# Performance work log

Hardware: AMD Instinct MI355X
Metric: run time of the kernel (lower is better)

The kernel has to match this reference:

```python
import jax, jax.numpy as jnp
import numpy as np

N = 100000        # nodes
E = 1600000       # directed edges (before self loops)
F = 128           # input node features
H1, H2, H3 = 64, 32, 16
G = 64            # graphs in batch
EPS = 1e-5
NEG_SLOPE = 0.2


def setup_inputs():
    key = jax.random.key(0)
    ks = jax.random.split(key, 16)
    def rn(k, shape, scale=1.0):
        return jax.random.normal(k, shape, dtype=jnp.float32) * scale
    inp = {}
    inp['x'] = rn(ks[0], (N, F))
    inp['edge_index'] = jax.random.randint(ks[1], (2, E), 0, N)
    inp['batch'] = jnp.sort(jax.random.randint(ks[2], (N,), 0, G))
    dims = [(F, H1), (H1, H2), (H2, H3)]
    i = 3
    for li, (fi, fo) in enumerate(dims, start=1):
        s = 1.0 / np.sqrt(fi)
        kk = jax.random.split(ks[i], 3)
        inp[f'Wl{li}'] = rn(kk[0], (fi, fo), s)
        inp[f'bl{li}'] = jnp.zeros((fo,), jnp.float32)
        inp[f'Wr{li}'] = rn(kk[1], (fi, fo), s)
        inp[f'br{li}'] = jnp.zeros((fo,), jnp.float32)
        inp[f'att{li}'] = rn(kk[2], (fo,), 1.0 / np.sqrt(fo))
        inp[f'bias{li}'] = jnp.zeros((fo,), jnp.float32)
        inp[f'gamma{li}'] = jnp.ones((fo,), jnp.float32)
        inp[f'beta{li}'] = jnp.zeros((fo,), jnp.float32)
        i += 1
    inp['linW'] = rn(ks[i], (H3, 1), 0.25)
    inp['linb'] = jnp.zeros((1,), jnp.float32)
    return inp


def _gatv2(x, Wl, bl, Wr, br, att, bias, src, dst):
    # PyG GATv2Conv, heads=1: e_ij = a^T LeakyReLU(Wl x_j + Wr x_i)
    xl = x @ Wl + bl                         # [N, H] source transform
    xr = x @ Wr + br                         # [N, H] target transform
    e = jax.nn.leaky_relu(xl[src] + xr[dst], NEG_SLOPE) @ att   # [E']
    # numerically stable segment softmax over incoming edges of dst
    emax = jax.ops.segment_max(e, dst, num_segments=N)
    w = jnp.exp(e - emax[dst])
    denom = jax.ops.segment_sum(w, dst, num_segments=N)
    alpha = w / (denom[dst] + 1e-16)         # [E']
    out = jax.ops.segment_sum(alpha[:, None] * xl[src], dst, num_segments=N)
    return out + bias


def _batchnorm(x, gamma, beta):
    mu = jnp.mean(x, axis=0)
    var = jnp.var(x, axis=0)
    return (x - mu) * jax.lax.rsqrt(var + EPS) * gamma + beta


def reference(x, edge_index, batch,
              Wl1, bl1, Wr1, br1, att1, bias1, gamma1, beta1,
              Wl2, bl2, Wr2, br2, att2, bias2, gamma2, beta2,
              Wl3, bl3, Wr3, br3, att3, bias3, gamma3, beta3,
              linW, linb):
    # add self loops once (PyG GATv2Conv default add_self_loops=True)
    loops = jnp.arange(N, dtype=edge_index.dtype)
    src = jnp.concatenate([edge_index[0], loops])
    dst = jnp.concatenate([edge_index[1], loops])

    h = _gatv2(x, Wl1, bl1, Wr1, br1, att1, bias1, src, dst)
    h = jax.nn.relu(_batchnorm(h, gamma1, beta1))
    h = _gatv2(h, Wl2, bl2, Wr2, br2, att2, bias2, src, dst)
    h = jax.nn.relu(_batchnorm(h, gamma2, beta2))
    h = _gatv2(h, Wl3, bl3, Wr3, br3, att3, bias3, src, dst)
    h = jax.nn.relu(_batchnorm(h, gamma3, beta3))

    # global mean pool over graphs
    sums = jax.ops.segment_sum(h, batch, num_segments=G)          # [G, 16]
    cnts = jax.ops.segment_sum(jnp.ones((N,), h.dtype), batch, num_segments=G)
    pooled = sums / jnp.maximum(cnts, 1.0)[:, None]
    return pooled @ linW + linb                                   # [G, 1]
```

## Files before the change

kernel.cpp:

```cpp
#include <hip/hip_runtime.h>
#include <hip/hip_bf16.h>


static constexpr int G_ = 64;

__global__ __launch_bounds__(256) void pack_w(
    const float* __restrict__ Wl, const float* __restrict__ Wr,
    const float* __restrict__ bl, const float* __restrict__ br,
    float* __restrict__ Wcat, float* __restrict__ bcat, int FI, int H) {
  int i = blockIdx.x * 256 + threadIdx.x;
  int FO = 2 * H;
  if (i < FI * FO) {
    int k = i / FO, c = i % FO;
    Wcat[i] = (c < H) ? Wl[k * H + c] : Wr[k * H + (c - H)];
  }
  if (i < FO) bcat[i] = (i < H) ? bl[i] : br[i - H];
}

template <int FI>
__global__ __launch_bounds__(256) void transpose_nf(
    const float* __restrict__ A, float* __restrict__ At, int N) {
  __shared__ float s[64][65];
  int n0 = blockIdx.x * 64, k0 = blockIdx.y * 64;
  int tid = threadIdx.x;
  for (int idx = tid; idx < 64 * 16; idx += 256) {
    int n = idx >> 4, c = idx & 15;
    float4 v = make_float4(0.f, 0.f, 0.f, 0.f);
    if (n0 + n < N)
      v = *reinterpret_cast<const float4*>(&A[(size_t)(n0 + n) * FI + k0 + c * 4]);
    s[n][c * 4 + 0] = v.x; s[n][c * 4 + 1] = v.y;
    s[n][c * 4 + 2] = v.z; s[n][c * 4 + 3] = v.w;
  }
  __syncthreads();
  for (int idx = tid; idx < 64 * 16; idx += 256) {
    int k = idx >> 4, c = idx & 15;
    int n = c * 4;
    if (n0 + n + 3 < N) {
      float4 v = make_float4(s[n][k], s[n + 1][k], s[n + 2][k], s[n + 3][k]);
      *reinterpret_cast<float4*>(&At[(size_t)(k0 + k) * N + n0 + n]) = v;
    } else {
      for (int j = 0; j < 4; j++)
        if (n0 + n + j < N) At[(size_t)(k0 + k) * N + n0 + n + j] = s[n + j][k];
    }
  }
}

__global__ __launch_bounds__(256) void edge_hist(
    const int* __restrict__ ei, int* __restrict__ deg, int E, int Etot, int N) {
  int p = blockIdx.x & 7;
  int q = blockIdx.x >> 3;
  int nbq = gridDim.x >> 3;
  float scale = 8.0f / (float)N;
  for (int i = q * 256 + threadIdx.x; i < Etot; i += nbq * 256) {
    int dst = (i < E) ? ei[E + i] : (i - E);
    int pp = min((int)((float)dst * scale), 7);
    if (pp == p) atomicAdd(&deg[dst], 1);
  }
}

__global__ __launch_bounds__(256) void scan1(
    const int* __restrict__ deg, int* __restrict__ part, int* __restrict__ bsums, int n) {
  __shared__ int ts[256];
  int t = threadIdx.x, b = blockIdx.x;
  int base = b * 1024 + t * 4;
  int d[4];
#pragma unroll
  for (int q = 0; q < 4; q++) d[q] = (base + q < n) ? deg[base + q] : 0;
  int s = d[0] + d[1] + d[2] + d[3];
  ts[t] = s;
  __syncthreads();
  for (int o = 1; o < 256; o <<= 1) {
    int v = (t >= o) ? ts[t - o] : 0;
    __syncthreads();
    ts[t] += v;
    __syncthreads();
  }
  int incl = ts[t];
  if (t == 255) bsums[b] = incl;
  int run = incl - s;
#pragma unroll
  for (int q = 0; q < 4; q++) {
    if (base + q < n) part[base + q] = run;
    run += d[q];
  }
}

__global__ void scan2(int* bsums, int nb) {
  if (threadIdx.x == 0 && blockIdx.x == 0) {
    int r = 0;
    for (int i = 0; i < nb; i++) { int t = bsums[i]; bsums[i] = r; r += t; }
  }
}

__global__ __launch_bounds__(256) void scan3(
    int* __restrict__ rp, int* __restrict__ cur, const int* __restrict__ bsums,
    int n, int Etot) {
  int i = blockIdx.x * 256 + threadIdx.x;
  if (i < n) {
    int v = rp[i] + bsums[i >> 10];
    rp[i] = v; cur[i] = v;
  }
  if (i == 0) rp[n] = Etot;
}

__global__ __launch_bounds__(256) void scatter_edges(
    const int* __restrict__ ei, int* __restrict__ cur, int* __restrict__ ssrc,
    int E, int Etot, int N) {
  int p = blockIdx.x & 7;
  int q = blockIdx.x >> 3;
  int nbq = gridDim.x >> 3;
  float scale = 8.0f / (float)N;
  for (int i = q * 256 + threadIdx.x; i < Etot; i += nbq * 256) {
    int dst = (i < E) ? ei[E + i] : (i - E);
    int pp = min((int)((float)dst * scale), 7);
    if (pp != p) continue;
    int src = (i < E) ? ei[i] : (i - E);
    int pos = atomicAdd(&cur[dst], 1);
    ssrc[pos] = src;
  }
}

template <int FI, int FO>
__global__ __launch_bounds__(256) void gemm_fmaj(
    const float* __restrict__ At, const float* __restrict__ Wcat,
    const float* __restrict__ bcat, float* __restrict__ C, int N) {
  constexpr int KC = 32;
  constexpr int HP = FO / 16;
  __shared__ float As[FI * 64];
  __shared__ float Ws[KC * FO];
  int tid = threadIdx.x;
  int ng = tid & 15, hg = tid >> 4;
  int n0 = blockIdx.x * 64;

  if (n0 + 64 <= N) {
    for (int idx = tid; idx < FI * 16; idx += 256) {
      int k = idx >> 4, c = idx & 15;
      *reinterpret_cast<float4*>(&As[k * 64 + c * 4]) =
          *reinterpret_cast<const float4*>(&At[(size_t)k * N + n0 + c * 4]);
    }
  } else {
    for (int idx = tid; idx < FI * 64; idx += 256) {
      int k = idx >> 6, nn = idx & 63;
      As[k * 64 + nn] = (n0 + nn < N) ? At[(size_t)k * N + n0 + nn] : 0.f;
    }
  }

  float acc[4][HP];
#pragma unroll
  for (int i = 0; i < 4; i++)
#pragma unroll
    for (int j = 0; j < HP; j++) acc[i][j] = 0.f;

  for (int kc = 0; kc < FI; kc += KC) {
    __syncthreads();
    for (int idx = tid; idx < KC * FO / 4; idx += 256)
      *reinterpret_cast<float4*>(&Ws[idx * 4]) =
          *reinterpret_cast<const float4*>(&Wcat[kc * FO + idx * 4]);
    __syncthreads();
#pragma unroll
    for (int kk = 0; kk < KC; kk++) {
      float a_[4];
#pragma unroll
      for (int i = 0; i < 4; i++) a_[i] = As[(kc + kk) * 64 + ng * 4 + i];
      float w_[HP];
#pragma unroll
      for (int j = 0; j < HP; j++) w_[j] = Ws[kk * FO + hg * HP + j];
#pragma unroll
      for (int i = 0; i < 4; i++)
#pragma unroll
        for (int j = 0; j < HP; j++) acc[i][j] += a_[i] * w_[j];
    }
  }

#pragma unroll
  for (int i = 0; i < 4; i++) {
    int n = n0 + ng * 4 + i;
    if (n < N) {
#pragma unroll
      for (int j = 0; j < HP; j++)
        C[(size_t)n * FO + hg * HP + j] = acc[i][j] + bcat[hg * HP + j];
    }
  }
}

__device__ __forceinline__ float lrelu02(float z) {
  return (z > 0.f) ? z : 0.2f * z;
}

template <int H, bool UN2>
__global__ __launch_bounds__(256) void gat_agg2(
    const float* __restrict__ xlr, const float* __restrict__ att,
    const float* __restrict__ bias, const int* __restrict__ rp,
    const int* __restrict__ ssrc, float* __restrict__ out, int N) {
  constexpr int L = H / 4;
  constexpr int C = 64 / L;
  int v = blockIdx.x * 4 + (threadIdx.x >> 6);
  if (v >= N) return;
  int lane = threadIdx.x & 63;
  int fl = lane % L;
  int sub = lane / L;

  const float4 xr4 = *reinterpret_cast<const float4*>(&xlr[(size_t)v * (2 * H) + H + fl * 4]);
  const float4 a4 = *reinterpret_cast<const float4*>(&att[fl * 4]);
  int beg = rp[v], end = rp[v + 1];

  float mA = -3.0e38f, dA = 0.f;
  float4 accA = make_float4(0.f, 0.f, 0.f, 0.f);
  float mB = -3.0e38f, dB = 0.f;
  float4 accB = make_float4(0.f, 0.f, 0.f, 0.f);

  constexpr int STEP = UN2 ? 2 * C : C;

  for (int j = beg + sub; j < end; j += STEP) {
    {
      int u = ssrc[j];
      float4 xl4 = *reinterpret_cast<const float4*>(&xlr[(size_t)u * (2 * H) + fl * 4]);
      float t = a4.x * lrelu02(xl4.x + xr4.x);
      t = fmaf(a4.y, lrelu02(xl4.y + xr4.y), t);
      t = fmaf(a4.z, lrelu02(xl4.z + xr4.z), t);
      t = fmaf(a4.w, lrelu02(xl4.w + xr4.w), t);
#pragma unroll
      for (int o = L / 2; o >= 1; o >>= 1) t += __shfl_xor(t, o);
      float mn = fmaxf(mA, t);
      float sc = __expf(mA - mn);
      float w = __expf(t - mn);
      dA = dA * sc + w;
      accA.x = fmaf(w, xl4.x, accA.x * sc);
      accA.y = fmaf(w, xl4.y, accA.y * sc);
      accA.z = fmaf(w, xl4.z, accA.z * sc);
      accA.w = fmaf(w, xl4.w, accA.w * sc);
      mA = mn;
    }
    if (UN2) {
      int j2 = j + C;
      if (j2 < end) {
        int u = ssrc[j2];
        float4 xl4 = *reinterpret_cast<const float4*>(&xlr[(size_t)u * (2 * H) + fl * 4]);
        float t = a4.x * lrelu02(xl4.x + xr4.x);
        t = fmaf(a4.y, lrelu02(xl4.y + xr4.y), t);
        t = fmaf(a4.z, lrelu02(xl4.z + xr4.z), t);
        t = fmaf(a4.w, lrelu02(xl4.w + xr4.w), t);
#pragma unroll
        for (int o = L / 2; o >= 1; o >>= 1) t += __shfl_xor(t, o);
        float mn = fmaxf(mB, t);
        float sc = __expf(mB - mn);
        float w = __expf(t - mn);
        dB = dB * sc + w;
        accB.x = fmaf(w, xl4.x, accB.x * sc);
        accB.y = fmaf(w, xl4.y, accB.y * sc);
        accB.z = fmaf(w, xl4.z, accB.z * sc);
        accB.w = fmaf(w, xl4.w, accB.w * sc);
        mB = mn;
      }
    }
  }

  if (UN2) {
    float mn = fmaxf(mA, mB);
    float s1 = __expf(mA - mn), s2 = __expf(mB - mn);
    dA = dA * s1 + dB * s2;
    accA.x = accA.x * s1 + accB.x * s2;
    accA.y = accA.y * s1 + accB.y * s2;
    accA.z = accA.z * s1 + accB.z * s2;
    accA.w = accA.w * s1 + accB.w * s2;
    mA = mn;
  }

#pragma unroll
  for (int o = L; o < 64; o <<= 1) {
    float mo = __shfl_xor(mA, o);
    float d2 = __shfl_xor(dA, o);
    float ax = __shfl_xor(accA.x, o);
    float ay = __shfl_xor(accA.y, o);
    float az = __shfl_xor(accA.z, o);
    float aw = __shfl_xor(accA.w, o);
    float mn = fmaxf(mA, mo);
    float s1 = __expf(mA - mn), s2 = __expf(mo - mn);
    dA = dA * s1 + d2 * s2;
    accA.x = accA.x * s1 + ax * s2;
    accA.y = accA.y * s1 + ay * s2;
    accA.z = accA.z * s1 + az * s2;
    accA.w = accA.w * s1 + aw * s2;
    mA = mn;
  }

  if (lane < L) {
    float inv = 1.f / (dA + 1e-16f);
    const float4 b4 = *reinterpret_cast<const float4*>(&bias[fl * 4]);
    float4 o4 = make_float4(fmaf(accA.x, inv, b4.x), fmaf(accA.y, inv, b4.y),
                            fmaf(accA.z, inv, b4.z), fmaf(accA.w, inv, b4.w));
    *reinterpret_cast<float4*>(&out[(size_t)v * H + fl * 4]) = o4;
  }
}

template <int H>
__global__ __launch_bounds__(256) void bn_stats(
    const float* __restrict__ X, float* __restrict__ stats, int N) {
  __shared__ float ls[256], ls2[256];
  int tid = threadIdx.x;
  int h = tid % H;
  constexpr int RPB = 256 / H;
  int r0 = blockIdx.x * RPB + tid / H;
  float s = 0.f, s2 = 0.f;
  for (int n = r0; n < N; n += gridDim.x * RPB) {
    float val = X[(size_t)n * H + h];
    s += val; s2 += val * val;
  }
  ls[tid] = s; ls2[tid] = s2;
  __syncthreads();
  if (tid < H) {
    for (int g = 1; g < RPB; g++) { s += ls[tid + g * H]; s2 += ls2[tid + g * H]; }
    atomicAdd(&stats[h], s);
    atomicAdd(&stats[H + h], s2);
  }
}

__global__ void bn_finalize(
    const float* __restrict__ stats, const float* __restrict__ gamma,
    const float* __restrict__ beta, float* __restrict__ ss, int H, int N) {
  int h = threadIdx.x;
  if (h < H) {
    float mean = stats[h] / (float)N;
    float var = stats[H + h] / (float)N - mean * mean;
    float istd = rsqrtf(var + 1e-5f);
    float sc = gamma[h] * istd;
    ss[h] = sc;
    ss[H + h] = beta[h] - mean * sc;
  }
}

template <int H>
__global__ __launch_bounds__(256) void bn_apply_T(
    const float* __restrict__ X, const float* __restrict__ ss,
    float* __restrict__ Yt, int N) {
  __shared__ float s[64][65];
  int n0 = blockIdx.x * 64;
  int tid = threadIdx.x;
  for (int idx = tid; idx < 64 * (H / 4); idx += 256) {
    int n = idx / (H / 4), c = idx % (H / 4);
    float4 v = make_float4(0.f, 0.f, 0.f, 0.f);
    if (n0 + n < N)
      v = *reinterpret_cast<const float4*>(&X[(size_t)(n0 + n) * H + c * 4]);
    s[n][c * 4 + 0] = v.x; s[n][c * 4 + 1] = v.y;
    s[n][c * 4 + 2] = v.z; s[n][c * 4 + 3] = v.w;
  }
  __syncthreads();
  for (int idx = tid; idx < H * 16; idx += 256) {
    int k = idx >> 4, c = idx & 15;
    int n = c * 4;
    float sc = ss[k], sh = ss[H + k];
    float t0 = s[n + 0][k] * sc + sh;
    float t1 = s[n + 1][k] * sc + sh;
    float t2 = s[n + 2][k] * sc + sh;
    float t3 = s[n + 3][k] * sc + sh;
    float4 v = make_float4(t0 > 0.f ? t0 : 0.f, t1 > 0.f ? t1 : 0.f,
                           t2 > 0.f ? t2 : 0.f, t3 > 0.f ? t3 : 0.f);
    if (n0 + n + 3 < N) {
      *reinterpret_cast<float4*>(&Yt[(size_t)k * N + n0 + n]) = v;
    } else {
      float tv[4] = {v.x, v.y, v.z, v.w};
      for (int j = 0; j < 4; j++)
        if (n0 + n + j < N) Yt[(size_t)k * N + n0 + n + j] = tv[j];
    }
  }
}

__global__ __launch_bounds__(256) void bn_apply_flat(
    const float* __restrict__ X, const float* __restrict__ ss,
    float* __restrict__ Y, int total) {
  int i = blockIdx.x * 256 + threadIdx.x;
  if (i < total) {
    int h = i & 15;
    float t = X[i] * ss[h] + ss[16 + h];
    Y[i] = t > 0.f ? t : 0.f;
  }
}

__global__ __launch_bounds__(256) void pool_kernel(
    const float* __restrict__ X, const int* __restrict__ batch,
    float* __restrict__ pool, float* __restrict__ cnt, int N) {
  __shared__ float lp[G_ * 16];
  __shared__ float lc[G_];
  int tid = threadIdx.x;
  for (int j = tid; j < G_ * 16; j += 256) lp[j] = 0.f;
  if (tid < G_) lc[tid] = 0.f;
  __syncthreads();
  int tot = N * 16;
  for (int i = blockIdx.x * 256 + tid; i < tot; i += gridDim.x * 256) {
    int n = i >> 4, h = i & 15;
    int g = batch[n];
    atomicAdd(&lp[g * 16 + h], X[i]);
    if (h == 0) atomicAdd(&lc[g], 1.0f);
  }
  __syncthreads();
  for (int j = tid; j < G_ * 16; j += 256) atomicAdd(&pool[j], lp[j]);
  if (tid < G_) atomicAdd(&cnt[tid], lc[tid]);
}

__global__ void final_linear(
    const float* __restrict__ pool, const float* __restrict__ cnt,
    const float* __restrict__ linW, const float* __restrict__ linb,
    float* __restrict__ out) {
  int g = threadIdx.x;
  if (g < G_) {
    float c = fmaxf(cnt[g], 1.0f);
    float acc = 0.f;
    for (int h = 0; h < 16; h++) acc += (pool[g * 16 + h] / c) * linW[h];
    out[g] = acc + linb[0];
  }
}

extern "C" void kernel_launch(void* const* d_in, const int* in_sizes, int n_in,
                              void* d_out, int out_size, void* d_ws, size_t ws_size,
                              hipStream_t stream) {
  const float* x = (const float*)d_in[0];
  const int* ei = (const int*)d_in[1];
  const int* batch = (const int*)d_in[2];
  const int N = in_sizes[0] / 128;
  const int E = in_sizes[1] / 2;
  const int Etot = E + N;

  char* wsb = (char*)d_ws;
  size_t off = 0;
  auto alloc = [&](size_t bytes) -> void* {
    void* p = wsb + off;
    off += (bytes + 255) & ~(size_t)255;
    return p;
  };
  float* R0 = (float*)alloc((size_t)128 * N * 4);
  float* R1 = (float*)alloc((size_t)128 * N * 4);
  float* R2 = (float*)alloc((size_t)64 * N * 4);
  int* deg = (int*)alloc((size_t)N * 4);
  int* row_ptr = (int*)alloc((size_t)(N + 1) * 4);
  int* cursor = (int*)alloc((size_t)N * 4);
  int* bsums = (int*)alloc(4096);
  int* ssrc = (int*)alloc((size_t)Etot * 4);
  float* Wc1 = (float*)alloc(16384 * 4);  float* bc1 = (float*)alloc(128 * 4);
  float* Wc2 = (float*)alloc(4096 * 4);   float* bc2 = (float*)alloc(64 * 4);
  float* Wc3 = (float*)alloc(1024 * 4);   float* bc3 = (float*)alloc(32 * 4);
  float* stats = (float*)alloc(128 * 4);
  float* ss = (float*)alloc(128 * 4);
  float* pool = (float*)alloc((G_ * 16 + G_) * 4);
  float* cnt = pool + G_ * 16;

  const float* Wl1 = (const float*)d_in[3];  const float* bl1 = (const float*)d_in[4];
  const float* Wr1 = (const float*)d_in[5];  const float* br1 = (const float*)d_in[6];
  const float* att1 = (const float*)d_in[7]; const float* bias1 = (const float*)d_in[8];
  const float* g1 = (const float*)d_in[9];   const float* b1 = (const float*)d_in[10];
  const float* Wl2 = (const float*)d_in[11]; const float* bl2 = (const float*)d_in[12];
  const float* Wr2 = (const float*)d_in[13]; const float* br2 = (const float*)d_in[14];
  const float* att2 = (const float*)d_in[15]; const float* bias2 = (const float*)d_in[16];
  const float* g2 = (const float*)d_in[17];  const float* b2 = (const float*)d_in[18];
  const float* Wl3 = (const float*)d_in[19]; const float* bl3 = (const float*)d_in[20];
  const float* Wr3 = (const float*)d_in[21]; const float* br3 = (const float*)d_in[22];
  const float* att3 = (const float*)d_in[23]; const float* bias3 = (const float*)d_in[24];
  const float* g3 = (const float*)d_in[25];  const float* b3 = (const float*)d_in[26];
  const float* linW = (const float*)d_in[27]; const float* linb = (const float*)d_in[28];
  float* out = (float*)d_out;

  int ntiles = (N + 63) / 64;
  int nb = (N + 1023) / 1024;
  int nnodeblk = (N + 3) / 4;

  pack_w<<<64, 256, 0, stream>>>(Wl1, Wr1, bl1, br1, Wc1, bc1, 128, 64);
  pack_w<<<16, 256, 0, stream>>>(Wl2, Wr2, bl2, br2, Wc2, bc2, 64, 32);
  pack_w<<<4, 256, 0, stream>>>(Wl3, Wr3, bl3, br3, Wc3, bc3, 32, 16);

  transpose_nf<128><<<dim3(ntiles, 2), 256, 0, stream>>>(x, R0, N);

  hipMemsetAsync(deg, 0, (size_t)N * 4, stream);
  edge_hist<<<4096, 256, 0, stream>>>(ei, deg, E, Etot, N);
  scan1<<<nb, 256, 0, stream>>>(deg, row_ptr, bsums, N);
  scan2<<<1, 64, 0, stream>>>(bsums, nb);
  scan3<<<(N + 255) / 256, 256, 0, stream>>>(row_ptr, cursor, bsums, N, Etot);
  scatter_edges<<<4096, 256, 0, stream>>>(ei, cursor, ssrc, E, Etot, N);

  gemm_fmaj<128, 128><<<ntiles, 256, 0, stream>>>(R0, Wc1, bc1, R1, N);
  gat_agg2<64, true><<<nnodeblk, 256, 0, stream>>>(R1, att1, bias1, row_ptr, ssrc, R2, N);
  hipMemsetAsync(stats, 0, 128 * 4, stream);
  bn_stats<64><<<512, 256, 0, stream>>>(R2, stats, N);
  bn_finalize<<<1, 64, 0, stream>>>(stats, g1, b1, ss, 64, N);
  bn_apply_T<64><<<ntiles, 256, 0, stream>>>(R2, ss, R0, N);

  gemm_fmaj<64, 64><<<ntiles, 256, 0, stream>>>(R0, Wc2, bc2, R1, N);
  gat_agg2<32, true><<<nnodeblk, 256, 0, stream>>>(R1, att2, bias2, row_ptr, ssrc, R2, N);
  hipMemsetAsync(stats, 0, 128 * 4, stream);
  bn_stats<32><<<512, 256, 0, stream>>>(R2, stats, N);
  bn_finalize<<<1, 64, 0, stream>>>(stats, g2, b2, ss, 32, N);
  bn_apply_T<32><<<ntiles, 256, 0, stream>>>(R2, ss, R0, N);

  gemm_fmaj<32, 32><<<ntiles, 256, 0, stream>>>(R0, Wc3, bc3, R1, N);
  gat_agg2<16, false><<<nnodeblk, 256, 0, stream>>>(R1, att3, bias3, row_ptr, ssrc, R2, N);
  hipMemsetAsync(stats, 0, 128 * 4, stream);
  bn_stats<16><<<512, 256, 0, stream>>>(R2, stats, N);
  bn_finalize<<<1, 64, 0, stream>>>(stats, g3, b3, ss, 16, N);
  bn_apply_flat<<<(N * 16 + 255) / 256, 256, 0, stream>>>(R2, ss, R0, N * 16);

  hipMemsetAsync(pool, 0, (G_ * 16 + G_) * 4, stream);
  pool_kernel<<<2048, 256, 0, stream>>>(R0, batch, pool, cnt, N);
  final_linear<<<1, 64, 0, stream>>>(pool, cnt, linW, linb, out);
}
```

Baseline: 610.1 us.

## Retile node GEMM to 128 rows per block and use lazy softmax rescaling

The feature GEMM now covers 128 nodes per block with 8 rows per thread, streams the A operand in K chunks through shared memory, and reads it as float4. This raises register reuse and cuts the shared-memory footprint. Separately, the online softmax in the aggregation kernels only rescales the running accumulators when a new score exceeds the running max by more than 8, which drops one exp and several multiplies per edge in the common case. The lazy rescale lets exponent terms grow up to e^8, a small numerical-range risk, and the larger GEMM tile halves the number of blocks.

```diff
diff --git a/kernel.cpp b/kernel.cpp
--- a/kernel.cpp
+++ b/kernel.cpp
@@ -121,64 +121,73 @@
 }
 
 template <int FI, int FO>
-__global__ __launch_bounds__(256) void gemm_fmaj(
+__global__ __launch_bounds__(256) void gemm_fmaj2(
     const float* __restrict__ At, const float* __restrict__ Wcat,
     const float* __restrict__ bcat, float* __restrict__ C, int N) {
   constexpr int KC = 32;
-  constexpr int HP = FO / 16;
-  __shared__ float As[FI * 64];
+  constexpr int CT = FO / 16;
+  __shared__ float As[KC * 128];
   __shared__ float Ws[KC * FO];
   int tid = threadIdx.x;
-  int ng = tid & 15, hg = tid >> 4;
-  int n0 = blockIdx.x * 64;
-
-  if (n0 + 64 <= N) {
-    for (int idx = tid; idx < FI * 16; idx += 256) {
-      int k = idx >> 4, c = idx & 15;
-      *reinterpret_cast<float4*>(&As[k * 64 + c * 4]) =
-          *reinterpret_cast<const float4*>(&At[(size_t)k * N + n0 + c * 4]);
-    }
-  } else {
-    for (int idx = tid; idx < FI * 64; idx += 256) {
-      int k = idx >> 6, nn = idx & 63;
-      As[k * 64 + nn] = (n0 + nn < N) ? At[(size_t)k * N + n0 + nn] : 0.f;
-    }
-  }
-
-  float acc[4][HP];
-#pragma unroll
-  for (int i = 0; i < 4; i++)
-#pragma unroll
-    for (int j = 0; j < HP; j++) acc[i][j] = 0.f;
+  int ng = tid & 15;
+  int hg = tid >> 4;
+  int n0 = blockIdx.x * 128;
+  bool full = (n0 + 128 <= N);
+
+  float acc[8][CT];
+#pragma unroll
+  for (int i = 0; i < 8; i++)
+#pragma unroll
+    for (int j = 0; j < CT; j++) acc[i][j] = 0.f;
 
   for (int kc = 0; kc < FI; kc += KC) {
     __syncthreads();
+    {
+      int r = tid >> 5;
+      int c = (tid & 31) * 4;
+      for (int rr = r; rr < KC; rr += 8) {
+        float4 v;
+        if (full) {
+          v = *reinterpret_cast<const float4*>(&At[(size_t)(kc + rr) * N + n0 + c]);
+        } else {
+          float tmp[4];
+#pragma unroll
+          for (int j = 0; j < 4; j++)
+            tmp[j] = (n0 + c + j < N) ? At[(size_t)(kc + rr) * N + n0 + c + j] : 0.f;
+          v = make_float4(tmp[0], tmp[1], tmp[2], tmp[3]);
+        }
+        *reinterpret_cast<float4*>(&As[rr * 128 + c]) = v;
+      }
+    }
     for (int idx = tid; idx < KC * FO / 4; idx += 256)
       *reinterpret_cast<float4*>(&Ws[idx * 4]) =
           *reinterpret_cast<const float4*>(&Wcat[kc * FO + idx * 4]);
     __syncthreads();
 #pragma unroll
     for (int kk = 0; kk < KC; kk++) {
-      float a_[4];
-#pragma unroll
-      for (int i = 0; i < 4; i++) a_[i] = As[(kc + kk) * 64 + ng * 4 + i];
-      float w_[HP];
-#pragma unroll
-      for (int j = 0; j < HP; j++) w_[j] = Ws[kk * FO + hg * HP + j];
-#pragma unroll
-      for (int i = 0; i < 4; i++)
-#pragma unroll
-        for (int j = 0; j < HP; j++) acc[i][j] += a_[i] * w_[j];
-    }
-  }
-
-#pragma unroll
-  for (int i = 0; i < 4; i++) {
-    int n = n0 + ng * 4 + i;
+      float4 alo = *reinterpret_cast<float4*>(&As[kk * 128 + 4 * ng]);
+      float4 ahi = *reinterpret_cast<float4*>(&As[kk * 128 + 64 + 4 * ng]);
+      float a[8] = {alo.x, alo.y, alo.z, alo.w, ahi.x, ahi.y, ahi.z, ahi.w};
+      float w[CT];
+#pragma unroll
+      for (int j = 0; j < CT; j++) w[j] = Ws[kk * FO + hg * CT + j];
+#pragma unroll
+      for (int i = 0; i < 8; i++)
+#pragma unroll
+        for (int j = 0; j < CT; j++) acc[i][j] = fmaf(a[i], w[j], acc[i][j]);
+    }
+  }
+
+  float b[CT];
+#pragma unroll
+  for (int j = 0; j < CT; j++) b[j] = bcat[hg * CT + j];
+#pragma unroll
+  for (int i = 0; i < 8; i++) {
+    int n = n0 + ((i < 4) ? (4 * ng + i) : (64 + 4 * ng + (i - 4)));
     if (n < N) {
 #pragma unroll
-      for (int j = 0; j < HP; j++)
-        C[(size_t)n * FO + hg * HP + j] = acc[i][j] + bcat[hg * HP + j];
+      for (int j = 0; j < CT; j++)
+        C[(size_t)n * FO + hg * CT + j] = acc[i][j] + b[j];
     }
   }
 }
@@ -221,15 +230,19 @@
       t = fmaf(a4.w, lrelu02(xl4.w + xr4.w), t);
 #pragma unroll
       for (int o = L / 2; o >= 1; o >>= 1) t += __shfl_xor(t, o);
-      float mn = fmaxf(mA, t);
-      float sc = __expf(mA - mn);
-      float w = __expf(t - mn);
-      dA = dA * sc + w;
-      accA.x = fmaf(w, xl4.x, accA.x * sc);
-      accA.y = fmaf(w, xl4.y, accA.y * sc);
-      accA.z = fmaf(w, xl4.z, accA.z * sc);
-      accA.w = fmaf(w, xl4.w, accA.w * sc);
-      mA = mn;
+      float diff = t - mA;
+      if (diff > 8.f) {
+        float sc = __expf(-diff);
+        dA *= sc;
+        accA.x *= sc; accA.y *= sc; accA.z *= sc; accA.w *= sc;
+        mA = t; diff = 0.f;
+      }
+      float w = __expf(diff);
+      dA += w;
+      accA.x = fmaf(w, xl4.x, accA.x);
+      accA.y = fmaf(w, xl4.y, accA.y);
+      accA.z = fmaf(w, xl4.z, accA.z);
+      accA.w = fmaf(w, xl4.w, accA.w);
     }
     if (UN2) {
       int j2 = j + C;
@@ -242,15 +255,19 @@
         t = fmaf(a4.w, lrelu02(xl4.w + xr4.w), t);
 #pragma unroll
         for (int o = L / 2; o >= 1; o >>= 1) t += __shfl_xor(t, o);
-        float mn = fmaxf(mB, t);
-        float sc = __expf(mB - mn);
-        float w = __expf(t - mn);
-        dB = dB * sc + w;
-        accB.x = fmaf(w, xl4.x, accB.x * sc);
-        accB.y = fmaf(w, xl4.y, accB.y * sc);
-        accB.z = fmaf(w, xl4.z, accB.z * sc);
-        accB.w = fmaf(w, xl4.w, accB.w * sc);
-        mB = mn;
+        float diff = t - mB;
+        if (diff > 8.f) {
+          float sc = __expf(-diff);
+          dB *= sc;
+          accB.x *= sc; accB.y *= sc; accB.z *= sc; accB.w *= sc;
+          mB = t; diff = 0.f;
+        }
+        float w = __expf(diff);
+        dB += w;
+        accB.x = fmaf(w, xl4.x, accB.x);
+        accB.y = fmaf(w, xl4.y, accB.y);
+        accB.z = fmaf(w, xl4.z, accB.z);
+        accB.w = fmaf(w, xl4.w, accB.w);
       }
     }
   }
@@ -459,6 +476,7 @@
   float* out = (float*)d_out;
 
   int ntiles = (N + 63) / 64;
+  int ntiles2 = (N + 127) / 128;
   int nb = (N + 1023) / 1024;
   int nnodeblk = (N + 3) / 4;
 
@@ -475,21 +493,21 @@
   scan3<<<(N + 255) / 256, 256, 0, stream>>>(row_ptr, cursor, bsums, N, Etot);
   scatter_edges<<<4096, 256, 0, stream>>>(ei, cursor, ssrc, E, Etot, N);
 
-  gemm_fmaj<128, 128><<<ntiles, 256, 0, stream>>>(R0, Wc1, bc1, R1, N);
+  gemm_fmaj2<128, 128><<<ntiles2, 256, 0, stream>>>(R0, Wc1, bc1, R1, N);
   gat_agg2<64, true><<<nnodeblk, 256, 0, stream>>>(R1, att1, bias1, row_ptr, ssrc, R2, N);
   hipMemsetAsync(stats, 0, 128 * 4, stream);
   bn_stats<64><<<512, 256, 0, stream>>>(R2, stats, N);
   bn_finalize<<<1, 64, 0, stream>>>(stats, g1, b1, ss, 64, N);
   bn_apply_T<64><<<ntiles, 256, 0, stream>>>(R2, ss, R0, N);
 
-  gemm_fmaj<64, 64><<<ntiles, 256, 0, stream>>>(R0, Wc2, bc2, R1, N);
+  gemm_fmaj2<64, 64><<<ntiles2, 256, 0, stream>>>(R0, Wc2, bc2, R1, N);
   gat_agg2<32, true><<<nnodeblk, 256, 0, stream>>>(R1, att2, bias2, row_ptr, ssrc, R2, N);
   hipMemsetAsync(stats, 0, 128 * 4, stream);
   bn_stats<32><<<512, 256, 0, stream>>>(R2, stats, N);
   bn_finalize<<<1, 64, 0, stream>>>(stats, g2, b2, ss, 32, N);
   bn_apply_T<32><<<ntiles, 256, 0, stream>>>(R2, ss, R0, N);
 
-  gemm_fmaj<32, 32><<<ntiles, 256, 0, stream>>>(R0, Wc3, bc3, R1, N);
+  gemm_fmaj2<32, 32><<<ntiles2, 256, 0, stream>>>(R0, Wc3, bc3, R1, N);
   gat_agg2<16, false><<<nnodeblk, 256, 0, stream>>>(R1, att3, bias3, row_ptr, ssrc, R2, N);
   hipMemsetAsync(stats, 0, 128 * 4, stream);
   bn_stats<16><<<512, 256, 0, stream>>>(R2, stats, N);
```

After: 603.7 us. No clear change (-1.1%).
